# Kernel optimization log

Measured on AMD Instinct MI355X. Metric: run time of the kernel, lower is better.

The kernel has to match this reference:

```python
import jax, jax.numpy as jnp
import numpy as np

N = 50000          # num nodes
E = 800000         # num edges
D = 128            # dim_in == embed_dim
MAX_NODES = 4      # hard-coded in SortConv.__init__
EPS = 1e-5


def setup_inputs() -> dict:
    key = jax.random.key(0)
    ks = jax.random.split(key, 16)
    inp = {
        'x': jax.random.normal(ks[0], (N, D), jnp.float32),
        'edge_index': jax.random.randint(ks[1], (2, E), 0, N, jnp.int32),
    }
    for i in range(2):
        o = 2 + 6 * i
        W = jax.random.normal(ks[o], (D, D), jnp.float32) * (2.0 / (D + D)) ** 0.5
        W = W / jnp.linalg.norm(W, axis=1, keepdims=True)   # reset_parameters row-normalization
        inp[f'W{i}'] = W
        inp[f'b{i}'] = jnp.zeros((D,), jnp.float32)
        inp[f'cw{i}'] = jax.random.normal(ks[o + 1], (MAX_NODES,), jnp.float32) * (2.0 / (MAX_NODES + 1)) ** 0.5
        inp[f'cb{i}'] = jnp.zeros((1,), jnp.float32)
        inp[f'a{i}'] = jax.random.uniform(ks[o + 2], (1,), jnp.float32, -1.0, 1.0)  # LinearCombination scalar
        inp[f'g{i}'] = jnp.ones((D,), jnp.float32)
        inp[f'be{i}'] = jnp.zeros((D,), jnp.float32)
        inp[f'blank{i}'] = jnp.zeros((D,), jnp.float32)      # learnable blank vector
    return inp


def sort_conv(x, edge_index, blank, W, b, cw, cb, a):
    n, d = x.shape
    e = edge_index.shape[1]
    src, dst = edge_index[0], edge_index[1]
    msgs = x[src]                                            # [E, D] raw messages (lin_project not applied to messages)
    order = jnp.argsort(dst)                                 # stable sort by destination (index_sort)
    dst_s = dst[order]
    counts = jax.ops.segment_sum(jnp.ones((e,), jnp.int32), dst, num_segments=n + 1)
    starts = jnp.concatenate([jnp.zeros((1,), jnp.int32), jnp.cumsum(counts)[:-1].astype(jnp.int32)])
    pos = jnp.arange(e, dtype=jnp.int32) - starts[dst_s]     # rank within each neighborhood
    slot = jnp.where(pos < MAX_NODES, pos, MAX_NODES)        # overflow edges -> trash slot (to_dense_batch truncation)
    dense = jnp.zeros((n + 1, MAX_NODES + 1, d), x.dtype).at[dst_s, slot].set(msgs[order])
    mask = jnp.zeros((n + 1, MAX_NODES + 1), bool).at[dst_s, slot].set(True)
    dense, mask = dense[:, :MAX_NODES], mask[:, :MAX_NODES]  # [N+1, 4, D], [N+1, 4]
    blank_p = W @ blank + b                                  # lin_project applied only to blank vector
    filled = dense + (~mask)[..., None].astype(x.dtype) * blank_p
    srt = jnp.sort(filled, axis=1)                           # per-feature sort over neighbor slots
    out = jnp.einsum('nmd,m->nd', srt, cw) + cb              # vector collapse: Linear(max_nodes, 1)
    node_out, blank_new = out[:-1], out[-1]                  # last row = all-blank graph -> new blank
    return a * x + node_out, a * blank + blank_new           # LinearCombination combine (num_repeats=1)


def batch_norm(h, g, be):
    mu = h.mean(0)
    var = h.var(0)
    return (h - mu) / jnp.sqrt(var + EPS) * g + be


def reference(x, edge_index, W0, b0, cw0, cb0, a0, g0, be0, blank0,
              W1, b1, cw1, cb1, a1, g1, be1, blank1):
    layers = [(W0, b0, cw0, cb0, a0, g0, be0, blank0),
              (W1, b1, cw1, cb1, a1, g1, be1, blank1)]
    for (W, b, cw, cb, a, g, be, blank) in layers:
        h, _ = sort_conv(x, edge_index, blank, W, b, cw, cb, a)
        h = batch_norm(h, g, be)
        x = x + h                                            # residual connection
    return x
```

## Files before the change

kernel.cpp:

```cpp
#include <hip/hip_runtime.h>

constexpr int N_NODES = 50000;
constexpr int N_EDGES = 800000;
constexpr int DIM     = 128;
constexpr int DIM4    = DIM / 4;
constexpr float BN_EPS = 1e-5f;

constexpr int EMPTY = 0x7F7F7F7F;

constexpr int NC = 16;
constexpr int EC = 16;
constexpr int NODES_PER_NC = N_NODES / NC;
constexpr int EDGES_PER_EC = N_EDGES / EC;
constexpr int E4_PER_EC    = EDGES_PER_EC / 4;
constexpr int SEL_THREADS  = 1024;

constexpr int NBUCKETS = 16;
constexpr int ZERO_WORDS = 2 * NBUCKETS * 256;

constexpr int NB_MERGE = (N_NODES + 127) / 128;

constexpr int NODES_PER_ITER  = 8;
constexpr int NODES_PER_BLOCK = 16;
constexpr int CONV_GRID = N_NODES / NODES_PER_BLOCK;

__device__ inline float4 f4min(float4 a, float4 b) {
    return make_float4(fminf(a.x,b.x), fminf(a.y,b.y), fminf(a.z,b.z), fminf(a.w,b.w));
}
__device__ inline float4 f4max(float4 a, float4 b) {
    return make_float4(fmaxf(a.x,b.x), fmaxf(a.y,b.y), fmaxf(a.z,b.z), fmaxf(a.w,b.w));
}
__device__ inline float4 f4add(float4 a, float4 b) {
    return make_float4(a.x+b.x, a.y+b.y, a.z+b.z, a.w+b.w);
}
__device__ inline float4 f4fma(float s, float4 v, float4 acc) {
    return make_float4(fmaf(s,v.x,acc.x), fmaf(s,v.y,acc.y), fmaf(s,v.z,acc.z), fmaf(s,v.w,acc.w));
}

__global__ __launch_bounds__(SEL_THREADS)
void select_stageA_kernel(const int* __restrict__ dst,
                          int* __restrict__ tables) {
    __shared__ int slot[NODES_PER_NC * 4];
    const int nc = blockIdx.x & (NC - 1);
    const int ec = blockIdx.x >> 4;
    const int t  = threadIdx.x;

    for (int i = t; i < NODES_PER_NC * 4; i += SEL_THREADS) slot[i] = EMPTY;
    __syncthreads();

    const int r0 = nc * NODES_PER_NC;
    const int4* __restrict__ dst4 = (const int4*)dst;
    const int base4 = ec * E4_PER_EC;
    for (int i = t; i < E4_PER_EC; i += SEL_THREADS) {
        const int4 d = dst4[base4 + i];
        const int ebase = 4 * (base4 + i);
        #define TRY_INS(comp, off) {                                        \
            unsigned n_ = (unsigned)((comp) - r0);                          \
            if (n_ < (unsigned)NODES_PER_NC) {                              \
                int cur_ = ebase + (off);                                   \
                _Pragma("unroll")                                           \
                for (int j_ = 0; j_ < 4; ++j_) {                            \
                    int old_ = atomicMin(&slot[4 * n_ + j_], cur_);         \
                    if (old_ == EMPTY) break;                               \
                    cur_ = max(cur_, old_);                                 \
                } } }
        TRY_INS(d.x, 0); TRY_INS(d.y, 1); TRY_INS(d.z, 2); TRY_INS(d.w, 3);
        #undef TRY_INS
    }
    __syncthreads();

    int4* __restrict__ out = (int4*)tables + (size_t)ec * N_NODES + r0;
    const int4* __restrict__ sl4 = (const int4*)slot;
    for (int n = t; n < NODES_PER_NC; n += SEL_THREADS) out[n] = sl4[n];
}

__global__ __launch_bounds__(256)
void select_stageB_kernel(const int* __restrict__ tables,
                          const int* __restrict__ src,
                          int4* __restrict__ srcs4,
                          float* __restrict__ stats_part,
                          const float* __restrict__ W0, const float* __restrict__ b0,
                          const float* __restrict__ bl0,
                          const float* __restrict__ W1, const float* __restrict__ b1,
                          const float* __restrict__ bl1,
                          float* __restrict__ bp) {
    const int t = threadIdx.x;

    if (blockIdx.x >= NB_MERGE) {
        if (t < DIM) {
            int l = blockIdx.x - NB_MERGE;
            const float* W  = l ? W1  : W0;
            const float* b  = l ? b1  : b0;
            const float* bl = l ? bl1 : bl0;
            float s = 0.f;
            #pragma unroll 8
            for (int j = 0; j < DIM; ++j) s += W[t * DIM + j] * bl[j];
            bp[l * DIM + t] = s + b[t];
        }
        return;
    }

    const int gid = blockIdx.x * 256 + t;
    if (gid < ZERO_WORDS) stats_part[gid] = 0.f;

    const int vloc = t & 127;
    const int half = t >> 7;
    int v = blockIdx.x * 128 + vloc;
    const bool valid = (v < N_NODES);
    if (!valid) v = N_NODES - 1;

    int4 c[8];
    #pragma unroll
    for (int j = 0; j < 8; ++j)
        c[j] = ((const int4*)tables)[(size_t)(half * 8 + j) * N_NODES + v];

    int a0 = c[0].x, a1 = c[0].y, a2 = c[0].z, a3 = c[0].w;
    #define MERGE4(cx, cy, cz, cw) {                                 \
        int m0 = min(a0, (cw)), m1 = min(a1, (cz));                  \
        int m2 = min(a2, (cy)), m3 = min(a3, (cx));                  \
        int u_;                                                      \
        u_ = min(m0, m2); m2 = max(m0, m2); m0 = u_;                 \
        u_ = min(m1, m3); m3 = max(m1, m3); m1 = u_;                 \
        u_ = min(m0, m1); m1 = max(m0, m1); m0 = u_;                 \
        u_ = min(m2, m3); m3 = max(m2, m3); m2 = u_;                 \
        a0 = m0; a1 = m1; a2 = m2; a3 = m3; }
    #pragma unroll
    for (int j = 1; j < 8; ++j) MERGE4(c[j].x, c[j].y, c[j].z, c[j].w);

    __shared__ int4 xbuf[128];
    if (half) xbuf[vloc] = make_int4(a0, a1, a2, a3);
    __syncthreads();
    if (!half) {
        const int4 o = xbuf[vloc];
        MERGE4(o.x, o.y, o.z, o.w);
        int4 r;
        r.x = (a0 < N_EDGES) ? src[a0] : -1;
        r.y = (a1 < N_EDGES) ? src[a1] : -1;
        r.z = (a2 < N_EDGES) ? src[a2] : -1;
        r.w = (a3 < N_EDGES) ? src[a3] : -1;
        if (valid) srcs4[v] = r;
    }
    #undef MERGE4
}

__global__ __launch_bounds__(256)
void conv_stats_kernel(const float* __restrict__ x,
                       const int4* __restrict__ srcs4,
                       const float* __restrict__ bp,
                       const float* __restrict__ cw,
                       const float* __restrict__ cb,
                       const float* __restrict__ a,
                       float* __restrict__ h,
                       float* __restrict__ stats_part) {
    const int t    = threadIdx.x;
    const int d4   = t & (DIM4 - 1);
    const int nsub = t >> 5;

    const float4* __restrict__ x4 = (const float4*)x;
    float4*       __restrict__ h4 = (float4*)h;

    const float aa = a[0];
    const float c0 = cw[0], c1 = cw[1], c2 = cw[2], c3 = cw[3];
    const float cbv = cb[0];
    const float4 bpv = ((const float4*)bp)[d4];

    const int v0 = blockIdx.x * NODES_PER_BLOCK + nsub;
    const int v1 = v0 + NODES_PER_ITER;

    const int4 s0 = srcs4[v0];
    const int4 s1 = srcs4[v1];

    float4 g00 = x4[(size_t)max(s0.x, 0) * DIM4 + d4];
    float4 g01 = x4[(size_t)max(s0.y, 0) * DIM4 + d4];
    float4 g02 = x4[(size_t)max(s0.z, 0) * DIM4 + d4];
    float4 g03 = x4[(size_t)max(s0.w, 0) * DIM4 + d4];
    float4 g10 = x4[(size_t)max(s1.x, 0) * DIM4 + d4];
    float4 g11 = x4[(size_t)max(s1.y, 0) * DIM4 + d4];
    float4 g12 = x4[(size_t)max(s1.z, 0) * DIM4 + d4];
    float4 g13 = x4[(size_t)max(s1.w, 0) * DIM4 + d4];
    float4 xv0 = x4[(size_t)v0 * DIM4 + d4];
    float4 xv1 = x4[(size_t)v1 * DIM4 + d4];

    float4 s  = make_float4(0.f, 0.f, 0.f, 0.f);
    float4 s2 = make_float4(0.f, 0.f, 0.f, 0.f);

    #define CSWAP4(p, q) { float4 lo = f4min(p, q); float4 hi = f4max(p, q); p = lo; q = hi; }
    {
        float4 m0 = (s0.x >= 0) ? g00 : bpv;
        float4 m1 = (s0.y >= 0) ? g01 : bpv;
        float4 m2 = (s0.z >= 0) ? g02 : bpv;
        float4 m3 = (s0.w >= 0) ? g03 : bpv;
        CSWAP4(m0, m1); CSWAP4(m2, m3); CSWAP4(m0, m2); CSWAP4(m1, m3); CSWAP4(m1, m2);
        float4 hv = make_float4(cbv, cbv, cbv, cbv);
        hv = f4fma(c0, m0, hv);
        hv = f4fma(c1, m1, hv);
        hv = f4fma(c2, m2, hv);
        hv = f4fma(c3, m3, hv);
        hv = f4fma(aa, xv0, hv);
        h4[(size_t)v0 * DIM4 + d4] = hv;
        s  = f4add(s, hv);
        s2 = f4add(s2, make_float4(hv.x*hv.x, hv.y*hv.y, hv.z*hv.z, hv.w*hv.w));
    }
    {
        float4 m0 = (s1.x >= 0) ? g10 : bpv;
        float4 m1 = (s1.y >= 0) ? g11 : bpv;
        float4 m2 = (s1.z >= 0) ? g12 : bpv;
        float4 m3 = (s1.w >= 0) ? g13 : bpv;
        CSWAP4(m0, m1); CSWAP4(m2, m3); CSWAP4(m0, m2); CSWAP4(m1, m3); CSWAP4(m1, m2);
        float4 hv = make_float4(cbv, cbv, cbv, cbv);
        hv = f4fma(c0, m0, hv);
        hv = f4fma(c1, m1, hv);
        hv = f4fma(c2, m2, hv);
        hv = f4fma(c3, m3, hv);
        hv = f4fma(aa, xv1, hv);
        h4[(size_t)v1 * DIM4 + d4] = hv;
        s  = f4add(s, hv);
        s2 = f4add(s2, make_float4(hv.x*hv.x, hv.y*hv.y, hv.z*hv.z, hv.w*hv.w));
    }
    #undef CSWAP4

    s.x  += __shfl_down(s.x, 32);  s.y  += __shfl_down(s.y, 32);
    s.z  += __shfl_down(s.z, 32);  s.w  += __shfl_down(s.w, 32);
    s2.x += __shfl_down(s2.x, 32); s2.y += __shfl_down(s2.y, 32);
    s2.z += __shfl_down(s2.z, 32); s2.w += __shfl_down(s2.w, 32);

    __shared__ float4 ls[4][32];
    __shared__ float4 ls2[4][32];
    const int wave = t >> 6;
    const int lane = t & 63;
    if (lane < 32) { ls[wave][lane] = s; ls2[wave][lane] = s2; }
    __syncthreads();
    if (t < 32) {
        float* bucket = stats_part + (size_t)(blockIdx.x & (NBUCKETS - 1)) * 256;
        float4 fs  = f4add(f4add(ls[0][t],  ls[1][t]),  f4add(ls[2][t],  ls[3][t]));
        float4 fs2 = f4add(f4add(ls2[0][t], ls2[1][t]), f4add(ls2[2][t], ls2[3][t]));
        atomicAdd(&bucket[4*t + 0], fs.x);
        atomicAdd(&bucket[4*t + 1], fs.y);
        atomicAdd(&bucket[4*t + 2], fs.z);
        atomicAdd(&bucket[4*t + 3], fs.w);
        atomicAdd(&bucket[DIM + 4*t + 0], fs2.x);
        atomicAdd(&bucket[DIM + 4*t + 1], fs2.y);
        atomicAdd(&bucket[DIM + 4*t + 2], fs2.z);
        atomicAdd(&bucket[DIM + 4*t + 3], fs2.w);
    }
}

__global__ __launch_bounds__(256)
void bn_apply_kernel(const float* __restrict__ xin,
                     const float* __restrict__ h,
                     const float* __restrict__ stats_part,
                     const float* __restrict__ g,
                     const float* __restrict__ be,
                     float* __restrict__ xout) {
    __shared__ float acc[256];
    const int t = threadIdx.x;

    float ssum = 0.f;
    #pragma unroll
    for (int k = 0; k < NBUCKETS; ++k) ssum += stats_part[k * 256 + t];
    acc[t] = ssum;
    __syncthreads();
    if (t < 128) {
        constexpr float invN = 1.0f / (float)N_NODES;
        float mu = acc[t] * invN;
        float iv = rsqrtf(acc[128 + t] * invN - mu * mu + BN_EPS);
        acc[t]       = mu;
        acc[128 + t] = iv;
    }
    __syncthreads();

    const int idx = blockIdx.x * 256 + t;
    const int d4 = idx & (DIM4 - 1);

    const float4 mu4 = make_float4(acc[4*d4+0], acc[4*d4+1], acc[4*d4+2], acc[4*d4+3]);
    const float4 iv4 = make_float4(acc[128+4*d4+0], acc[128+4*d4+1],
                                   acc[128+4*d4+2], acc[128+4*d4+3]);
    const float4 hv = ((const float4*)h)[idx];
    const float4 xv = ((const float4*)xin)[idx];
    const float4 gv = ((const float4*)g)[d4];
    const float4 bv = ((const float4*)be)[d4];

    float4 o;
    o.x = xv.x + (hv.x - mu4.x) * iv4.x * gv.x + bv.x;
    o.y = xv.y + (hv.y - mu4.y) * iv4.y * gv.y + bv.y;
    o.z = xv.z + (hv.z - mu4.z) * iv4.z * gv.z + bv.z;
    o.w = xv.w + (hv.w - mu4.w) * iv4.w * gv.w + bv.w;
    ((float4*)xout)[idx] = o;
}

extern "C" void kernel_launch(void* const* d_in, const int* in_sizes, int n_in,
                              void* d_out, int out_size, void* d_ws, size_t ws_size,
                              hipStream_t stream) {
    const float* x0  = (const float*)d_in[0];
    const int*   ei  = (const int*)d_in[1];
    const int*   src = ei;
    const int*   dst = ei + N_EDGES;

    const float* W[2]; const float* b[2]; const float* cw[2]; const float* cb[2];
    const float* a[2]; const float* g[2]; const float* be[2]; const float* blank[2];
    for (int i = 0; i < 2; ++i) {
        int o = 2 + 8 * i;
        W[i]     = (const float*)d_in[o + 0];
        b[i]     = (const float*)d_in[o + 1];
        cw[i]    = (const float*)d_in[o + 2];
        cb[i]    = (const float*)d_in[o + 3];
        a[i]     = (const float*)d_in[o + 4];
        g[i]     = (const float*)d_in[o + 5];
        be[i]    = (const float*)d_in[o + 6];
        blank[i] = (const float*)d_in[o + 7];
    }

    char* ws = (char*)d_ws;
    int*   srcs       = (int*)ws;
    float* h          = (float*)(srcs + 4 * N_NODES);
    int*   tables     = (int*)h;
    float* stats_part = h + (size_t)N_NODES * DIM;
    float* bp         = stats_part + ZERO_WORDS;

    float* xout = (float*)d_out;

    select_stageA_kernel<<<NC * EC, SEL_THREADS, 0, stream>>>(dst, tables);
    select_stageB_kernel<<<NB_MERGE + 2, 256, 0, stream>>>(
        tables, src, (int4*)srcs, stats_part,
        W[0], b[0], blank[0], W[1], b[1], blank[1], bp);

    for (int l = 0; l < 2; ++l) {
        const float* xin = (l == 0) ? x0 : xout;
        float* sp = stats_part + (size_t)l * NBUCKETS * 256;
        conv_stats_kernel<<<CONV_GRID, 256, 0, stream>>>(
            xin, (const int4*)srcs, bp + l * DIM, cw[l], cb[l], a[l], h, sp);
        bn_apply_kernel<<<(N_NODES * DIM4) / 256, 256, 0, stream>>>(
            xin, h, sp, g[l], be[l], xout);
    }
}
```

Baseline: 207.2 us.

## Replace two-stage shared-memory edge selection with single global-atomic insertion table

The old path had each of 256 blocks scan a slice of edges, keep partial 4-smallest tables for a node range in shared memory, then merged 16 partial tables per node. It now does one pass over all edges with global atomicMin insertion into a per-node 4-slot table, initialised by a memset, and skips the atomics early when slot 3 already holds a smaller index. This removes the 16x redundant scan of dst and the merge stage. In exchange it relies on global atomics contending across the device, and the unsynchronised read of slot 3 is only a pruning hint.

```diff
diff --git a/kernel.cpp b/kernel.cpp
--- a/kernel.cpp
+++ b/kernel.cpp
@@ -8,17 +8,13 @@
 
 constexpr int EMPTY = 0x7F7F7F7F;
 
-constexpr int NC = 16;
-constexpr int EC = 16;
-constexpr int NODES_PER_NC = N_NODES / NC;
-constexpr int EDGES_PER_EC = N_EDGES / EC;
-constexpr int E4_PER_EC    = EDGES_PER_EC / 4;
-constexpr int SEL_THREADS  = 1024;
-
 constexpr int NBUCKETS = 16;
 constexpr int ZERO_WORDS = 2 * NBUCKETS * 256;
 
-constexpr int NB_MERGE = (N_NODES + 127) / 128;
+constexpr int NB_MAP = (N_NODES + 255) / 256;
+
+constexpr int SCAN_THREADS = 256;
+constexpr int SCAN_GRID = (N_EDGES / 4 + SCAN_THREADS - 1) / SCAN_THREADS;
 
 constexpr int NODES_PER_ITER  = 8;
 constexpr int NODES_PER_BLOCK = 16;
@@ -37,58 +33,47 @@
     return make_float4(fmaf(s,v.x,acc.x), fmaf(s,v.y,acc.y), fmaf(s,v.z,acc.z), fmaf(s,v.w,acc.w));
 }
 
-__global__ __launch_bounds__(SEL_THREADS)
-void select_stageA_kernel(const int* __restrict__ dst,
-                          int* __restrict__ tables) {
-    __shared__ int slot[NODES_PER_NC * 4];
-    const int nc = blockIdx.x & (NC - 1);
-    const int ec = blockIdx.x >> 4;
-    const int t  = threadIdx.x;
-
-    for (int i = t; i < NODES_PER_NC * 4; i += SEL_THREADS) slot[i] = EMPTY;
-    __syncthreads();
-
-    const int r0 = nc * NODES_PER_NC;
-    const int4* __restrict__ dst4 = (const int4*)dst;
-    const int base4 = ec * E4_PER_EC;
-    for (int i = t; i < E4_PER_EC; i += SEL_THREADS) {
-        const int4 d = dst4[base4 + i];
-        const int ebase = 4 * (base4 + i);
-        #define TRY_INS(comp, off) {                                        \
-            unsigned n_ = (unsigned)((comp) - r0);                          \
-            if (n_ < (unsigned)NODES_PER_NC) {                              \
-                int cur_ = ebase + (off);                                   \
-                _Pragma("unroll")                                           \
-                for (int j_ = 0; j_ < 4; ++j_) {                            \
-                    int old_ = atomicMin(&slot[4 * n_ + j_], cur_);         \
-                    if (old_ == EMPTY) break;                               \
-                    cur_ = max(cur_, old_);                                 \
-                } } }
-        TRY_INS(d.x, 0); TRY_INS(d.y, 1); TRY_INS(d.z, 2); TRY_INS(d.w, 3);
-        #undef TRY_INS
-    }
-    __syncthreads();
-
-    int4* __restrict__ out = (int4*)tables + (size_t)ec * N_NODES + r0;
-    const int4* __restrict__ sl4 = (const int4*)slot;
-    for (int n = t; n < NODES_PER_NC; n += SEL_THREADS) out[n] = sl4[n];
+__global__ __launch_bounds__(SCAN_THREADS)
+void select_scan_kernel(const int* __restrict__ dst,
+                        int* __restrict__ gtab) {
+    const int gid = blockIdx.x * SCAN_THREADS + threadIdx.x;
+    if (gid >= N_EDGES / 4) return;
+    const int4 d = ((const int4*)dst)[gid];
+    const int ebase = 4 * gid;
+
+    #define INSERT(node, e) {                                               \
+        int* slot_ = gtab + 4 * (node);                                     \
+        int s3_ = slot_[3];                                                 \
+        if (s3_ >= (e)) {                                                   \
+            int cur_ = (e);                                                 \
+            _Pragma("unroll")                                               \
+            for (int j_ = 0; j_ < 4; ++j_) {                                \
+                int old_ = atomicMin(&slot_[j_], cur_);                     \
+                if (old_ == EMPTY) break;                                   \
+                cur_ = max(cur_, old_);                                     \
+            } } }
+    INSERT(d.x, ebase + 0);
+    INSERT(d.y, ebase + 1);
+    INSERT(d.z, ebase + 2);
+    INSERT(d.w, ebase + 3);
+    #undef INSERT
 }
 
 __global__ __launch_bounds__(256)
-void select_stageB_kernel(const int* __restrict__ tables,
-                          const int* __restrict__ src,
-                          int4* __restrict__ srcs4,
-                          float* __restrict__ stats_part,
-                          const float* __restrict__ W0, const float* __restrict__ b0,
-                          const float* __restrict__ bl0,
-                          const float* __restrict__ W1, const float* __restrict__ b1,
-                          const float* __restrict__ bl1,
-                          float* __restrict__ bp) {
+void select_map_kernel(const int* __restrict__ gtab,
+                       const int* __restrict__ src,
+                       int4* __restrict__ srcs4,
+                       float* __restrict__ stats_part,
+                       const float* __restrict__ W0, const float* __restrict__ b0,
+                       const float* __restrict__ bl0,
+                       const float* __restrict__ W1, const float* __restrict__ b1,
+                       const float* __restrict__ bl1,
+                       float* __restrict__ bp) {
     const int t = threadIdx.x;
 
-    if (blockIdx.x >= NB_MERGE) {
+    if (blockIdx.x >= NB_MAP) {
         if (t < DIM) {
-            int l = blockIdx.x - NB_MERGE;
+            int l = blockIdx.x - NB_MAP;
             const float* W  = l ? W1  : W0;
             const float* b  = l ? b1  : b0;
             const float* bl = l ? bl1 : bl0;
@@ -103,44 +88,14 @@
     const int gid = blockIdx.x * 256 + t;
     if (gid < ZERO_WORDS) stats_part[gid] = 0.f;
 
-    const int vloc = t & 127;
-    const int half = t >> 7;
-    int v = blockIdx.x * 128 + vloc;
-    const bool valid = (v < N_NODES);
-    if (!valid) v = N_NODES - 1;
-
-    int4 c[8];
-    #pragma unroll
-    for (int j = 0; j < 8; ++j)
-        c[j] = ((const int4*)tables)[(size_t)(half * 8 + j) * N_NODES + v];
-
-    int a0 = c[0].x, a1 = c[0].y, a2 = c[0].z, a3 = c[0].w;
-    #define MERGE4(cx, cy, cz, cw) {                                 \
-        int m0 = min(a0, (cw)), m1 = min(a1, (cz));                  \
-        int m2 = min(a2, (cy)), m3 = min(a3, (cx));                  \
-        int u_;                                                      \
-        u_ = min(m0, m2); m2 = max(m0, m2); m0 = u_;                 \
-        u_ = min(m1, m3); m3 = max(m1, m3); m1 = u_;                 \
-        u_ = min(m0, m1); m1 = max(m0, m1); m0 = u_;                 \
-        u_ = min(m2, m3); m3 = max(m2, m3); m2 = u_;                 \
-        a0 = m0; a1 = m1; a2 = m2; a3 = m3; }
-    #pragma unroll
-    for (int j = 1; j < 8; ++j) MERGE4(c[j].x, c[j].y, c[j].z, c[j].w);
-
-    __shared__ int4 xbuf[128];
-    if (half) xbuf[vloc] = make_int4(a0, a1, a2, a3);
-    __syncthreads();
-    if (!half) {
-        const int4 o = xbuf[vloc];
-        MERGE4(o.x, o.y, o.z, o.w);
-        int4 r;
-        r.x = (a0 < N_EDGES) ? src[a0] : -1;
-        r.y = (a1 < N_EDGES) ? src[a1] : -1;
-        r.z = (a2 < N_EDGES) ? src[a2] : -1;
-        r.w = (a3 < N_EDGES) ? src[a3] : -1;
-        if (valid) srcs4[v] = r;
-    }
-    #undef MERGE4
+    if (gid >= N_NODES) return;
+    const int4 c = ((const int4*)gtab)[gid];
+    int4 r;
+    r.x = (c.x < N_EDGES) ? src[c.x] : -1;
+    r.y = (c.y < N_EDGES) ? src[c.y] : -1;
+    r.z = (c.z < N_EDGES) ? src[c.z] : -1;
+    r.w = (c.w < N_EDGES) ? src[c.w] : -1;
+    srcs4[gid] = r;
 }
 
 __global__ __launch_bounds__(256)
@@ -312,16 +267,17 @@
 
     char* ws = (char*)d_ws;
     int*   srcs       = (int*)ws;
-    float* h          = (float*)(srcs + 4 * N_NODES);
-    int*   tables     = (int*)h;
+    int*   gtab       = srcs + 4 * N_NODES;
+    float* h          = (float*)(gtab + 4 * N_NODES);
     float* stats_part = h + (size_t)N_NODES * DIM;
     float* bp         = stats_part + ZERO_WORDS;
 
     float* xout = (float*)d_out;
 
-    select_stageA_kernel<<<NC * EC, SEL_THREADS, 0, stream>>>(dst, tables);
-    select_stageB_kernel<<<NB_MERGE + 2, 256, 0, stream>>>(
-        tables, src, (int4*)srcs, stats_part,
+    hipMemsetAsync(gtab, 0x7F, (size_t)4 * N_NODES * sizeof(int), stream);
+    select_scan_kernel<<<SCAN_GRID, SCAN_THREADS, 0, stream>>>(dst, gtab);
+    select_map_kernel<<<NB_MAP + 2, 256, 0, stream>>>(
+        gtab, src, (int4*)srcs, stats_part,
         W[0], b[0], blank[0], W[1], b[1], blank[1], bp);
 
     for (int l = 0; l < 2; ++l) {
```

Measured after the change: 296.4 us. +43.1%, slower.

## Fuse neighbor-table merge into first conv pass and store h as fp16

Applied to the files above, without the earlier changes.

Removes the separate stage-B merge kernel. The bias projection and stats zeroing move into extra blocks of stage A, and the 16-way table merge plus src lookup moves into the first conv_stats launch, which writes srcs for reuse by layer two. The intermediate h buffer is now stored as half precision and unpacked in bn_apply, halving that round-trip traffic. This saves one launch and memory bandwidth, but fp16 rounding of h adds precision error after BN normalization. Because h is stored rounded while the BN statistics are accumulated from the fp32 values, the normalized output can drift slightly.

```diff
diff --git a/kernel.cpp b/kernel.cpp
--- a/kernel.cpp
+++ b/kernel.cpp
@@ -1,4 +1,6 @@
 #include <hip/hip_runtime.h>
+#include <hip/hip_fp16.h>
+#include <cstring>
 
 constexpr int N_NODES = 50000;
 constexpr int N_EDGES = 800000;
@@ -18,8 +20,6 @@
 constexpr int NBUCKETS = 16;
 constexpr int ZERO_WORDS = 2 * NBUCKETS * 256;
 
-constexpr int NB_MERGE = (N_NODES + 127) / 128;
-
 constexpr int NODES_PER_ITER  = 8;
 constexpr int NODES_PER_BLOCK = 16;
 constexpr int CONV_GRID = N_NODES / NODES_PER_BLOCK;
@@ -36,14 +36,51 @@
 __device__ inline float4 f4fma(float s, float4 v, float4 acc) {
     return make_float4(fmaf(s,v.x,acc.x), fmaf(s,v.y,acc.y), fmaf(s,v.z,acc.z), fmaf(s,v.w,acc.w));
 }
+__device__ inline __half2 u2h2(unsigned u) { __half2 h; memcpy(&h, &u, 4); return h; }
+__device__ inline unsigned h22u(__half2 h) { unsigned u; memcpy(&u, &h, 4); return u; }
+__device__ inline float4 q2f4(uint2 q) {
+    const float2 lo = __half22float2(u2h2(q.x));
+    const float2 hi = __half22float2(u2h2(q.y));
+    return make_float4(lo.x, lo.y, hi.x, hi.y);
+}
+__device__ inline uint2 f42q(float4 v) {
+    uint2 u;
+    u.x = h22u(__floats2half2_rn(v.x, v.y));
+    u.y = h22u(__floats2half2_rn(v.z, v.w));
+    return u;
+}
 
 __global__ __launch_bounds__(SEL_THREADS)
 void select_stageA_kernel(const int* __restrict__ dst,
-                          int* __restrict__ tables) {
+                          int* __restrict__ tables,
+                          float* __restrict__ stats_part,
+                          const float* __restrict__ W0, const float* __restrict__ b0,
+                          const float* __restrict__ bl0,
+                          const float* __restrict__ W1, const float* __restrict__ b1,
+                          const float* __restrict__ bl1,
+                          float* __restrict__ bp) {
+    const int t = threadIdx.x;
+
+    if (blockIdx.x >= NC * EC) {
+        if (t < DIM) {
+            int l = blockIdx.x - NC * EC;
+            const float* W  = l ? W1  : W0;
+            const float* b  = l ? b1  : b0;
+            const float* bl = l ? bl1 : bl0;
+            float s = 0.f;
+            #pragma unroll 8
+            for (int j = 0; j < DIM; ++j) s += W[t * DIM + j] * bl[j];
+            bp[l * DIM + t] = s + b[t];
+        }
+        return;
+    }
+
+    const int gid = blockIdx.x * SEL_THREADS + t;
+    if (gid < ZERO_WORDS) stats_part[gid] = 0.f;
+
     __shared__ int slot[NODES_PER_NC * 4];
     const int nc = blockIdx.x & (NC - 1);
     const int ec = blockIdx.x >> 4;
-    const int t  = threadIdx.x;
 
     for (int i = t; i < NODES_PER_NC * 4; i += SEL_THREADS) slot[i] = EMPTY;
     __syncthreads();
@@ -75,100 +112,73 @@
 }
 
 __global__ __launch_bounds__(256)
-void select_stageB_kernel(const int* __restrict__ tables,
-                          const int* __restrict__ src,
-                          int4* __restrict__ srcs4,
-                          float* __restrict__ stats_part,
-                          const float* __restrict__ W0, const float* __restrict__ b0,
-                          const float* __restrict__ bl0,
-                          const float* __restrict__ W1, const float* __restrict__ b1,
-                          const float* __restrict__ bl1,
-                          float* __restrict__ bp) {
-    const int t = threadIdx.x;
-
-    if (blockIdx.x >= NB_MERGE) {
-        if (t < DIM) {
-            int l = blockIdx.x - NB_MERGE;
-            const float* W  = l ? W1  : W0;
-            const float* b  = l ? b1  : b0;
-            const float* bl = l ? bl1 : bl0;
-            float s = 0.f;
-            #pragma unroll 8
-            for (int j = 0; j < DIM; ++j) s += W[t * DIM + j] * bl[j];
-            bp[l * DIM + t] = s + b[t];
-        }
-        return;
-    }
-
-    const int gid = blockIdx.x * 256 + t;
-    if (gid < ZERO_WORDS) stats_part[gid] = 0.f;
-
-    const int vloc = t & 127;
-    const int half = t >> 7;
-    int v = blockIdx.x * 128 + vloc;
-    const bool valid = (v < N_NODES);
-    if (!valid) v = N_NODES - 1;
-
-    int4 c[8];
-    #pragma unroll
-    for (int j = 0; j < 8; ++j)
-        c[j] = ((const int4*)tables)[(size_t)(half * 8 + j) * N_NODES + v];
-
-    int a0 = c[0].x, a1 = c[0].y, a2 = c[0].z, a3 = c[0].w;
-    #define MERGE4(cx, cy, cz, cw) {                                 \
-        int m0 = min(a0, (cw)), m1 = min(a1, (cz));                  \
-        int m2 = min(a2, (cy)), m3 = min(a3, (cx));                  \
-        int u_;                                                      \
-        u_ = min(m0, m2); m2 = max(m0, m2); m0 = u_;                 \
-        u_ = min(m1, m3); m3 = max(m1, m3); m1 = u_;                 \
-        u_ = min(m0, m1); m1 = max(m0, m1); m0 = u_;                 \
-        u_ = min(m2, m3); m3 = max(m2, m3); m2 = u_;                 \
-        a0 = m0; a1 = m1; a2 = m2; a3 = m3; }
-    #pragma unroll
-    for (int j = 1; j < 8; ++j) MERGE4(c[j].x, c[j].y, c[j].z, c[j].w);
-
-    __shared__ int4 xbuf[128];
-    if (half) xbuf[vloc] = make_int4(a0, a1, a2, a3);
-    __syncthreads();
-    if (!half) {
-        const int4 o = xbuf[vloc];
-        MERGE4(o.x, o.y, o.z, o.w);
-        int4 r;
-        r.x = (a0 < N_EDGES) ? src[a0] : -1;
-        r.y = (a1 < N_EDGES) ? src[a1] : -1;
-        r.z = (a2 < N_EDGES) ? src[a2] : -1;
-        r.w = (a3 < N_EDGES) ? src[a3] : -1;
-        if (valid) srcs4[v] = r;
-    }
-    #undef MERGE4
-}
-
-__global__ __launch_bounds__(256)
 void conv_stats_kernel(const float* __restrict__ x,
-                       const int4* __restrict__ srcs4,
+                       const int* __restrict__ tables,
+                       const int* __restrict__ src,
+                       int4* __restrict__ srcs4,
                        const float* __restrict__ bp,
                        const float* __restrict__ cw,
                        const float* __restrict__ cb,
                        const float* __restrict__ a,
-                       float* __restrict__ h,
-                       float* __restrict__ stats_part) {
+                       uint2* __restrict__ h2,
+                       float* __restrict__ stats_part,
+                       const int do_merge) {
+    __shared__ int4 srcs_lds[NODES_PER_BLOCK];
+    __shared__ int4 tile[EC][NODES_PER_BLOCK];
+
     const int t    = threadIdx.x;
     const int d4   = t & (DIM4 - 1);
     const int nsub = t >> 5;
+    const int v0b  = blockIdx.x * NODES_PER_BLOCK;
+
+    if (do_merge) {
+        tile[t >> 4][t & 15] =
+            ((const int4*)tables)[(size_t)(t >> 4) * N_NODES + v0b + (t & 15)];
+        __syncthreads();
+        if (t < NODES_PER_BLOCK) {
+            int4 c = tile[0][t];
+            int a0 = c.x, a1 = c.y, a2 = c.z, a3 = c.w;
+            #define MERGE4(cx, cy, cz, cw_) {                            \
+                int m0 = min(a0, (cw_)), m1 = min(a1, (cz));             \
+                int m2 = min(a2, (cy)), m3 = min(a3, (cx));              \
+                int u_;                                                  \
+                u_ = min(m0, m2); m2 = max(m0, m2); m0 = u_;             \
+                u_ = min(m1, m3); m3 = max(m1, m3); m1 = u_;             \
+                u_ = min(m0, m1); m1 = max(m0, m1); m0 = u_;             \
+                u_ = min(m2, m3); m3 = max(m2, m3); m2 = u_;             \
+                a0 = m0; a1 = m1; a2 = m2; a3 = m3; }
+            #pragma unroll
+            for (int ec = 1; ec < EC; ++ec) {
+                c = tile[ec][t];
+                MERGE4(c.x, c.y, c.z, c.w);
+            }
+            #undef MERGE4
+            int4 r;
+            r.x = (a0 < N_EDGES) ? src[a0] : -1;
+            r.y = (a1 < N_EDGES) ? src[a1] : -1;
+            r.z = (a2 < N_EDGES) ? src[a2] : -1;
+            r.w = (a3 < N_EDGES) ? src[a3] : -1;
+            srcs_lds[t] = r;
+            srcs4[v0b + t] = r;
+        }
+        __syncthreads();
+    } else {
+        if (t < NODES_PER_BLOCK) srcs_lds[t] = srcs4[v0b + t];
+        __syncthreads();
+    }
 
     const float4* __restrict__ x4 = (const float4*)x;
-    float4*       __restrict__ h4 = (float4*)h;
 
     const float aa = a[0];
     const float c0 = cw[0], c1 = cw[1], c2 = cw[2], c3 = cw[3];
     const float cbv = cb[0];
     const float4 bpv = ((const float4*)bp)[d4];
 
-    const int v0 = blockIdx.x * NODES_PER_BLOCK + nsub;
+    const int v0 = v0b + nsub;
     const int v1 = v0 + NODES_PER_ITER;
 
-    const int4 s0 = srcs4[v0];
-    const int4 s1 = srcs4[v1];
+    const int4 s0 = srcs_lds[nsub];
+    const int4 s1 = srcs_lds[nsub + NODES_PER_ITER];
 
     float4 g00 = x4[(size_t)max(s0.x, 0) * DIM4 + d4];
     float4 g01 = x4[(size_t)max(s0.y, 0) * DIM4 + d4];
@@ -197,7 +207,7 @@
         hv = f4fma(c2, m2, hv);
         hv = f4fma(c3, m3, hv);
         hv = f4fma(aa, xv0, hv);
-        h4[(size_t)v0 * DIM4 + d4] = hv;
+        h2[(size_t)v0 * DIM4 + d4] = f42q(hv);
         s  = f4add(s, hv);
         s2 = f4add(s2, make_float4(hv.x*hv.x, hv.y*hv.y, hv.z*hv.z, hv.w*hv.w));
     }
@@ -213,7 +223,7 @@
         hv = f4fma(c2, m2, hv);
         hv = f4fma(c3, m3, hv);
         hv = f4fma(aa, xv1, hv);
-        h4[(size_t)v1 * DIM4 + d4] = hv;
+        h2[(size_t)v1 * DIM4 + d4] = f42q(hv);
         s  = f4add(s, hv);
         s2 = f4add(s2, make_float4(hv.x*hv.x, hv.y*hv.y, hv.z*hv.z, hv.w*hv.w));
     }
@@ -247,7 +257,7 @@
 
 __global__ __launch_bounds__(256)
 void bn_apply_kernel(const float* __restrict__ xin,
-                     const float* __restrict__ h,
+                     const uint2* __restrict__ h2,
                      const float* __restrict__ stats_part,
                      const float* __restrict__ g,
                      const float* __restrict__ be,
@@ -275,7 +285,7 @@
     const float4 mu4 = make_float4(acc[4*d4+0], acc[4*d4+1], acc[4*d4+2], acc[4*d4+3]);
     const float4 iv4 = make_float4(acc[128+4*d4+0], acc[128+4*d4+1],
                                    acc[128+4*d4+2], acc[128+4*d4+3]);
-    const float4 hv = ((const float4*)h)[idx];
+    const float4 hv = q2f4(h2[idx]);
     const float4 xv = ((const float4*)xin)[idx];
     const float4 gv = ((const float4*)g)[d4];
     const float4 bv = ((const float4*)be)[d4];
@@ -312,24 +322,24 @@
 
     char* ws = (char*)d_ws;
     int*   srcs       = (int*)ws;
-    float* h          = (float*)(srcs + 4 * N_NODES);
-    int*   tables     = (int*)h;
-    float* stats_part = h + (size_t)N_NODES * DIM;
+    int*   tables     = srcs + 4 * N_NODES;
+    uint2* h2         = (uint2*)(tables + (size_t)EC * 4 * N_NODES);
+    float* stats_part = (float*)(h2 + (size_t)N_NODES * DIM4);
     float* bp         = stats_part + ZERO_WORDS;
 
     float* xout = (float*)d_out;
 
-    select_stageA_kernel<<<NC * EC, SEL_THREADS, 0, stream>>>(dst, tables);
-    select_stageB_kernel<<<NB_MERGE + 2, 256, 0, stream>>>(
-        tables, src, (int4*)srcs, stats_part,
+    select_stageA_kernel<<<NC * EC + 2, SEL_THREADS, 0, stream>>>(
+        dst, tables, stats_part,
         W[0], b[0], blank[0], W[1], b[1], blank[1], bp);
 
     for (int l = 0; l < 2; ++l) {
         const float* xin = (l == 0) ? x0 : xout;
         float* sp = stats_part + (size_t)l * NBUCKETS * 256;
         conv_stats_kernel<<<CONV_GRID, 256, 0, stream>>>(
-            xin, (const int4*)srcs, bp + l * DIM, cw[l], cb[l], a[l], h, sp);
+            xin, tables, src, (int4*)srcs, bp + l * DIM,
+            cw[l], cb[l], a[l], h2, sp, (l == 0) ? 1 : 0);
         bn_apply_kernel<<<(N_NODES * DIM4) / 256, 256, 0, stream>>>(
-            xin, h, sp, g[l], be[l], xout);
-    }
-}
+            xin, h2, sp, g[l], be[l], xout);
+    }
+}
```

New measurement: 197.4 us. -4.7%, faster.
